# Kernel tuning notes

Hardware: AMD Instinct MI355X
Metric: run time of the kernel (lower is better)

## Reference

```python
import jax, jax.numpy as jnp
import numpy as np

# Dimensions (see shape_source): 28 indices per sample, values in [0, 8)
NX, NY, DIM, VOCAB = 2048, 2048, 28, 8
INTRA, INTER = 1.0, 2.0  # intra_class_distance, inter_class_distance
NCLS = 3
# index -> class id, derived from set_list = [[3,4,5,6],[0,1,2],[7]]
LUT = jnp.array([1, 1, 1, 0, 0, 0, 0, 2], dtype=jnp.int32)


def setup_inputs() -> dict:
    key = jax.random.key(0)
    k1, k2 = jax.random.split(key)
    return {
        "set_r": jax.random.randint(k1, (NX, DIM), 0, VOCAB, dtype=jnp.int32),
        "set_t": jax.random.randint(k2, (NY, DIM), 0, VOCAB, dtype=jnp.int32),
        "sigma": jnp.ones((), dtype=jnp.float32),
    }


def reference(set_r, set_t, sigma):
    # Per-position distance rule (from vector_distance, since set_list covers
    # every index exactly once):
    #   r == t                -> 0
    #   class(r) == class(t)  -> INTRA
    #   otherwise             -> INTER
    # sum over positions = INTRA*(cls_eq_cnt - eq_cnt) + INTER*(DIM - cls_eq_cnt)
    # Counts of matching positions are computed as one-hot GEMMs to avoid a
    # [NX, NY, DIM] intermediate.
    oh_r = jax.nn.one_hot(set_r, VOCAB, dtype=jnp.float32)       # [NX, DIM, V]
    oh_t = jax.nn.one_hot(set_t, VOCAB, dtype=jnp.float32)       # [NY, DIM, V]
    eq_cnt = jnp.einsum('idv,jdv->ij', oh_r, oh_t)               # [NX, NY]
    ch_r = jax.nn.one_hot(LUT[set_r], NCLS, dtype=jnp.float32)   # [NX, DIM, C]
    ch_t = jax.nn.one_hot(LUT[set_t], NCLS, dtype=jnp.float32)   # [NY, DIM, C]
    cls_cnt = jnp.einsum('idc,jdc->ij', ch_r, ch_t)              # [NX, NY]
    dist = (INTRA * (cls_cnt - eq_cnt) + INTER * (DIM - cls_cnt)) / DIM
    # Gaussain_kernel: exp(-d^2 / (2*sigma^2))
    return jnp.exp(-(dist ** 2) / (2.0 * sigma ** 2))
```

## Files before the change

### kernel.cpp

```cpp
#include <hip/hip_runtime.h>

#define NXD 2048
#define NYD 2048
#define DIMD 28
#define TI 32
#define TJ 128

#define CLS_TABLE 0x20000111u

__global__ __launch_bounds__(256) void setdist_kernel(
    const int* __restrict__ set_r,
    const int* __restrict__ set_t,
    const float* __restrict__ sigma_p,
    float* __restrict__ out)
{
    __shared__ unsigned long long r_pk[TI][6];
    __shared__ unsigned long long t_pk[TJ][6];

    const int tid = threadIdx.x;
    const int i0 = blockIdx.y * TI;
    const int j0 = blockIdx.x * TJ;

    if (tid < TI + TJ) {
        const bool isR = (tid < TI);
        const int row = isR ? (i0 + tid) : (j0 + (tid - TI));
        const int* src = (isR ? set_r : set_t) + row * DIMD;

        int vals[DIMD];
        const int4* s4 = (const int4*)src;
        #pragma unroll
        for (int q = 0; q < 7; ++q) {
            int4 w = s4[q];
            vals[4*q + 0] = w.x; vals[4*q + 1] = w.y;
            vals[4*q + 2] = w.z; vals[4*q + 3] = w.w;
        }

        unsigned long long eq0 = 0, eq1 = 0, eq2 = 0, eq3 = 0;
        unsigned long long cl0 = 0, cl1 = 0;
        #pragma unroll
        for (int d = 0; d < DIMD; ++d) {
            const int v = vals[d];
            const int b = d * 8 + v;
            const unsigned long long bit = 1ull << (b & 63);
            switch (b >> 6) {
                case 0: eq0 |= bit; break;
                case 1: eq1 |= bit; break;
                case 2: eq2 |= bit; break;
                default: eq3 |= bit; break;
            }
            const int c = (CLS_TABLE >> (4 * v)) & 0xF;
            const int bc = d * 4 + c;
            if (bc < 64) cl0 |= 1ull << bc;
            else         cl1 |= 1ull << (bc - 64);
        }
        unsigned long long* dst = isR ? r_pk[tid] : t_pk[tid - TI];
        dst[0] = eq0; dst[1] = eq1; dst[2] = eq2; dst[3] = eq3;
        dst[4] = cl0; dst[5] = cl1;
    }

    const float sg = sigma_p[0];
    const float k = 1.0f / (2.0f * sg * sg * 28.0f * 28.0f);

    __syncthreads();

    const int jj = tid & (TJ - 1);
    const int iBase = (tid >> 7) * 16;

    const unsigned long long te0 = t_pk[jj][0];
    const unsigned long long te1 = t_pk[jj][1];
    const unsigned long long te2 = t_pk[jj][2];
    const unsigned long long te3 = t_pk[jj][3];
    const unsigned long long tc0 = t_pk[jj][4];
    const unsigned long long tc1 = t_pk[jj][5];

    float* orow = out + (size_t)(i0 + iBase) * NYD + (j0 + jj);

    #pragma unroll
    for (int u = 0; u < 16; ++u) {
        const int il = iBase + u;
        const int s =
            __popcll(r_pk[il][0] & te0) + __popcll(r_pk[il][1] & te1) +
            __popcll(r_pk[il][2] & te2) + __popcll(r_pk[il][3] & te3) +
            __popcll(r_pk[il][4] & tc0) + __popcll(r_pk[il][5] & tc1);
        const float c = (float)(56 - s);
        orow[(size_t)u * NYD] = __expf(-c * c * k);
    }
}

extern "C" void kernel_launch(void* const* d_in, const int* in_sizes, int n_in,
                              void* d_out, int out_size, void* d_ws, size_t ws_size,
                              hipStream_t stream) {
    const int*   set_r = (const int*)d_in[0];
    const int*   set_t = (const int*)d_in[1];
    const float* sigma = (const float*)d_in[2];
    float*       out   = (float*)d_out;

    dim3 grid(NYD / TJ, NXD / TI);
    dim3 block(256);
    setdist_kernel<<<grid, block, 0, stream>>>(set_r, set_t, sigma, out);
}
```

Before: 71.24 us.

## Split bit-packing into a separate kernel and write float4 outputs per thread

Packing of one-hot bitmasks moves into a pre-pass kernel that writes 12-dword rows to workspace, so the main kernel no longer repacks rows per block and drops shared memory and the barrier. The class bits are compacted to 3 per position so they fit in fewer words. Each thread now handles 4 adjacent columns and stores float4 vectors, which widens the output writes on this write-bound 16 MB output. It adds a second launch and global reads of packed rows that are served from cache.

```diff
diff --git a/kernel.cpp b/kernel.cpp
--- a/kernel.cpp
+++ b/kernel.cpp
@@ -1,89 +1,103 @@
 #include <hip/hip_runtime.h>
+#include <stdint.h>
 
 #define NXD 2048
 #define NYD 2048
 #define DIMD 28
-#define TI 32
-#define TJ 128
+#define ROW_DW 12
 
 #define CLS_TABLE 0x20000111u
 
-__global__ __launch_bounds__(256) void setdist_kernel(
-    const int* __restrict__ set_r,
-    const int* __restrict__ set_t,
-    const float* __restrict__ sigma_p,
+
+__global__ __launch_bounds__(256) void pack_kernel(
+    const int* __restrict__ set_r, const int* __restrict__ set_t,
+    uint32_t* __restrict__ ws)
+{
+    const int row = blockIdx.x * 256 + threadIdx.x;
+    const int* src = (row < NXD) ? (set_r + row * DIMD)
+                                 : (set_t + (size_t)(row - NXD) * DIMD);
+    int vals[DIMD];
+    const int4* s4 = (const int4*)src;
+    #pragma unroll
+    for (int q = 0; q < 7; ++q) {
+        int4 v = s4[q];
+        vals[4*q+0] = v.x; vals[4*q+1] = v.y;
+        vals[4*q+2] = v.z; vals[4*q+3] = v.w;
+    }
+
+    unsigned long long e0 = 0, e1 = 0, e2 = 0, e3 = 0;
+    unsigned long long c0 = 0, c1 = 0;
+    #pragma unroll
+    for (int d = 0; d < DIMD; ++d) {
+        const int v = vals[d];
+        const int be = d * 8 + v;
+        const unsigned long long bit = 1ull << (be & 63);
+        switch (be >> 6) {
+            case 0: e0 |= bit; break;
+            case 1: e1 |= bit; break;
+            case 2: e2 |= bit; break;
+            default: e3 |= bit; break;
+        }
+        const int c = (CLS_TABLE >> (4 * v)) & 0xF;
+        const int bc = d * 3 + c;
+        if (bc < 64) c0 |= 1ull << bc;
+        else         c1 |= 1ull << (bc - 64);
+    }
+
+    uint32_t w0 = (uint32_t)e0, w1 = (uint32_t)(e0 >> 32);
+    uint32_t w2 = (uint32_t)e1, w3 = (uint32_t)(e1 >> 32);
+    uint32_t w4 = (uint32_t)e2, w5 = (uint32_t)(e2 >> 32);
+    uint32_t w6 = (uint32_t)e3;
+    uint32_t w7 = (uint32_t)c0, w8 = (uint32_t)(c0 >> 32);
+    uint32_t w9 = (uint32_t)c1;
+
+    uint4* dst = (uint4*)(ws + (size_t)row * ROW_DW);
+    dst[0] = make_uint4(w0, w1, w2, w3);
+    dst[1] = make_uint4(w4, w5, w6, w7);
+    dst[2] = make_uint4(w8, w9, 0u, 0u);
+}
+
+__global__ __launch_bounds__(256) void dist_kernel(
+    const uint32_t* __restrict__ ws, const float* __restrict__ sigma_p,
     float* __restrict__ out)
 {
-    __shared__ unsigned long long r_pk[TI][6];
-    __shared__ unsigned long long t_pk[TJ][6];
+    const int lane = threadIdx.x & 63;
+    const int wave = threadIdx.x >> 6;
+    const int i_base = blockIdx.y * 32 + wave * 8;
+    const int j_base = blockIdx.x * 256 + lane * 4;
 
-    const int tid = threadIdx.x;
-    const int i0 = blockIdx.y * TI;
-    const int j0 = blockIdx.x * TJ;
-
-    if (tid < TI + TJ) {
-        const bool isR = (tid < TI);
-        const int row = isR ? (i0 + tid) : (j0 + (tid - TI));
-        const int* src = (isR ? set_r : set_t) + row * DIMD;
-
-        int vals[DIMD];
-        const int4* s4 = (const int4*)src;
-        #pragma unroll
-        for (int q = 0; q < 7; ++q) {
-            int4 w = s4[q];
-            vals[4*q + 0] = w.x; vals[4*q + 1] = w.y;
-            vals[4*q + 2] = w.z; vals[4*q + 3] = w.w;
-        }
-
-        unsigned long long eq0 = 0, eq1 = 0, eq2 = 0, eq3 = 0;
-        unsigned long long cl0 = 0, cl1 = 0;
-        #pragma unroll
-        for (int d = 0; d < DIMD; ++d) {
-            const int v = vals[d];
-            const int b = d * 8 + v;
-            const unsigned long long bit = 1ull << (b & 63);
-            switch (b >> 6) {
-                case 0: eq0 |= bit; break;
-                case 1: eq1 |= bit; break;
-                case 2: eq2 |= bit; break;
-                default: eq3 |= bit; break;
-            }
-            const int c = (CLS_TABLE >> (4 * v)) & 0xF;
-            const int bc = d * 4 + c;
-            if (bc < 64) cl0 |= 1ull << bc;
-            else         cl1 |= 1ull << (bc - 64);
-        }
-        unsigned long long* dst = isR ? r_pk[tid] : t_pk[tid - TI];
-        dst[0] = eq0; dst[1] = eq1; dst[2] = eq2; dst[3] = eq3;
-        dst[4] = cl0; dst[5] = cl1;
+    const uint4* tp = (const uint4*)(ws + (size_t)(NXD + j_base) * ROW_DW);
+    uint4 T[4][3];
+    #pragma unroll
+    for (int s = 0; s < 4; ++s) {
+        T[s][0] = tp[s*3 + 0];
+        T[s][1] = tp[s*3 + 1];
+        T[s][2] = tp[s*3 + 2];
     }
 
     const float sg = sigma_p[0];
-    const float k = 1.0f / (2.0f * sg * sg * 28.0f * 28.0f);
+    const float k = 1.0f / (2.0f * sg * sg * (float)(DIMD * DIMD));
 
-    __syncthreads();
-
-    const int jj = tid & (TJ - 1);
-    const int iBase = (tid >> 7) * 16;
-
-    const unsigned long long te0 = t_pk[jj][0];
-    const unsigned long long te1 = t_pk[jj][1];
-    const unsigned long long te2 = t_pk[jj][2];
-    const unsigned long long te3 = t_pk[jj][3];
-    const unsigned long long tc0 = t_pk[jj][4];
-    const unsigned long long tc1 = t_pk[jj][5];
-
-    float* orow = out + (size_t)(i0 + iBase) * NYD + (j0 + jj);
-
+    const uint4* rp = (const uint4*)ws;
     #pragma unroll
-    for (int u = 0; u < 16; ++u) {
-        const int il = iBase + u;
-        const int s =
-            __popcll(r_pk[il][0] & te0) + __popcll(r_pk[il][1] & te1) +
-            __popcll(r_pk[il][2] & te2) + __popcll(r_pk[il][3] & te3) +
-            __popcll(r_pk[il][4] & tc0) + __popcll(r_pk[il][5] & tc1);
-        const float c = (float)(56 - s);
-        orow[(size_t)u * NYD] = __expf(-c * c * k);
+    for (int ii = 0; ii < 8; ++ii) {
+        const int i = i_base + ii;
+        const uint4 R0 = rp[i*3 + 0];
+        const uint4 R1 = rp[i*3 + 1];
+        const uint4 R2 = rp[i*3 + 2];
+        float4 res;
+        #pragma unroll
+        for (int s = 0; s < 4; ++s) {
+            const int sum =
+                __popc(R0.x & T[s][0].x) + __popc(R0.y & T[s][0].y) +
+                __popc(R0.z & T[s][0].z) + __popc(R0.w & T[s][0].w) +
+                __popc(R1.x & T[s][1].x) + __popc(R1.y & T[s][1].y) +
+                __popc(R1.z & T[s][1].z) + __popc(R1.w & T[s][1].w) +
+                __popc(R2.x & T[s][2].x) + __popc(R2.y & T[s][2].y);
+            const float c = (float)(56 - sum);
+            (&res.x)[s] = __expf(-c * c * k);
+        }
+        *(float4*)(out + (size_t)i * NYD + j_base) = res;
     }
 }
 
@@ -94,8 +108,9 @@
     const int*   set_t = (const int*)d_in[1];
     const float* sigma = (const float*)d_in[2];
     float*       out   = (float*)d_out;
+    uint32_t*    ws    = (uint32_t*)d_ws;
 
-    dim3 grid(NYD / TJ, NXD / TI);
-    dim3 block(256);
-    setdist_kernel<<<grid, block, 0, stream>>>(set_r, set_t, sigma, out);
+    pack_kernel<<<dim3((NXD + NYD) / 256), dim3(256), 0, stream>>>(set_r, set_t, ws);
+
+    dist_kernel<<<dim3(NYD / 256, NXD / 32), dim3(256), 0, stream>>>(ws, sigma, out);
 }
```

Result: slower. 73.20 us (+2.7%).
